# Optimization experiments

Hardware: AMD Instinct MI355X
Metric: run time of the kernel (lower is better)

Reference implementation:

```python
import jax, jax.numpy as jnp
import numpy as np
from jax import lax

BN_EPS = 1e-5
BNS = 1.0 / np.sqrt(1.0 + BN_EPS)  # eval-mode BatchNorm with mean=0, var=1, gamma=1, beta=0


def setup_inputs() -> dict:
    key = jax.random.key(0)
    ks = jax.random.split(key, 12)
    B, Cin, H, W = 8, 256, 128, 128
    NC, HD, RC, NL = 12, 64, 128, 3
    f = lambda k, shp, s: jax.random.normal(k, shp, jnp.float32) * s
    return dict(
        features=f(ks[0], (B, Cin, H, W), 1.0),
        segmentation=jax.random.uniform(ks[1], (B, NC, H, W), dtype=jnp.float32),
        W_rpn=f(ks[2], (RC, Cin, 3, 3), 0.02), b_rpn=jnp.zeros((RC,), jnp.float32),
        W_node=f(ks[3], (HD, RC), 0.08), b_node=jnp.zeros((HD,), jnp.float32),
        W_e1=f(ks[4], (2 * HD, HD), 0.08), b_e1=jnp.zeros((HD,), jnp.float32),
        W_e2=f(ks[5], (HD, HD), 0.1), b_e2=jnp.zeros((HD,), jnp.float32),
        W_g=f(ks[6], (NL, HD, HD), 0.1), b_g=jnp.zeros((NL, HD), jnp.float32),
        ln_g=jnp.ones((NL, HD), jnp.float32), ln_b=jnp.zeros((NL, HD), jnp.float32),
        glob_emb=f(ks[7], (NC, HD), 0.02),
        W_sp=f(ks[8], (HD, RC), 0.1), b_sp=jnp.zeros((RC,), jnp.float32),
    )


def _forward(features, segmentation, W_rpn, b_rpn, W_node, b_node, W_e1, b_e1,
             W_e2, b_e2, W_g, b_g, ln_g, ln_b, glob_emb, W_sp, b_sp):
    B, NC, H, W = segmentation.shape
    HD = W_node.shape[0]
    NL = W_g.shape[0]

    # ---- RegionProposalNetwork: 3x3 conv + BN(eval) + ReLU ----
    refined = lax.conv_general_dilated(
        features, W_rpn, (1, 1), 'SAME',
        dimension_numbers=('NCHW', 'OIHW', 'NCHW'))
    refined = jax.nn.relu((refined + b_rpn[None, :, None, None]) * BNS)  # [B,RC,H,W]

    # per-class 3x3 maxpool on segmentation, threshold -> binary masks
    pooled = lax.reduce_window(segmentation, -jnp.inf, lax.max,
                               (1, 1, 3, 3), (1, 1, 1, 1), 'SAME')
    masks = (pooled > 0.5).astype(features.dtype)  # [B,NC,H,W]

    # ---- NodeFeatureExtractor (1x1 conv is linear: conv(f*m)=(Wf)*m + b) ----
    yw = jnp.einsum('dk,bkhw->bdhw', W_node, refined)            # [B,HD,H,W]
    z = jax.nn.relu((yw + b_node[None, :, None, None]) * BNS)    # value inside mask region
    masked_sum = jnp.einsum('bdhw,bchw->bcd', z, masks)          # [B,NC,HD]
    mask_sum = masks.sum((2, 3))                                 # [B,NC]
    node_feats = masked_sum / (mask_sum[..., None] + 1e-6)       # [B,NC,HD]

    # ---- EdgeFeatureExtractor: all (i,j), i!=j, gated by class presence ----
    pairs = np.array([(i, j) for i in range(NC) for j in range(NC) if i != j])
    src = jnp.asarray(pairs[:, 0])  # [E]
    dst = jnp.asarray(pairs[:, 1])
    present = (mask_sum > 0).astype(features.dtype)              # [B,NC]
    valid = present[:, src] * present[:, dst]                    # [B,E]
    cat = jnp.concatenate([node_feats[:, src], node_feats[:, dst]], axis=-1)  # [B,E,2HD]
    h = jax.nn.relu(cat @ W_e1 + b_e1)
    edge_attr = (h @ W_e2 + b_e2) * valid[..., None]             # [B,E,HD]

    # ---- TissueGraphNetwork ----
    presence = (node_feats.sum(-1) != 0).astype(features.dtype)[..., None]  # [B,NC,1]
    seg_sum = jax.vmap(lambda m: jax.ops.segment_sum(m, dst, num_segments=NC))
    x = node_feats
    for l in range(NL):
        xw = x @ W_g[l]                                          # [B,NC,HD]
        msgs = xw[:, src] * edge_attr                            # [B,E,HD]
        agg = seg_sum(msgs) + b_g[l]
        xr = jax.nn.relu(agg)
        mu = xr.mean(-1, keepdims=True)
        var = ((xr - mu) ** 2).mean(-1, keepdims=True)
        normed = (xr - mu) / jnp.sqrt(var + 1e-5) * ln_g[l] + ln_b[l]
        x = normed + x if l > 0 else normed
    x = x * presence + glob_emb[None] * (1.0 - presence)         # [B,NC,HD]

    # ---- SpatialProjector ----
    spatial = jnp.einsum('bcd,bchw->bdhw', x, masks)             # [B,HD,H,W]
    out = jnp.einsum('do,bdhw->bohw', W_sp, spatial)             # [B,RC,H,W]
    out = jax.nn.relu((out + b_sp[None, :, None, None]) * BNS)
    return out


def reference(features, segmentation, W_rpn, b_rpn, W_node, b_node, W_e1, b_e1,
              W_e2, b_e2, W_g, b_g, ln_g, ln_b, glob_emb, W_sp, b_sp):
    return _forward(features, segmentation, W_rpn, b_rpn, W_node, b_node,
                    W_e1, b_e1, W_e2, b_e2, W_g, b_g, ln_g, ln_b,
                    glob_emb, W_sp, b_sp)
```

## Files before the change

kernel.cpp:

```cpp
#include <hip/hip_runtime.h>
#include <math.h>

#define BNS_F 0.9999950000374998f

typedef short short8 __attribute__((ext_vector_type(8)));
typedef float f32x16 __attribute__((ext_vector_type(16)));

typedef __attribute__((address_space(3))) void lds_void;
typedef const __attribute__((address_space(1))) void glb_void;

__device__ __forceinline__ unsigned short f2bf(float f) {
    unsigned u = __builtin_bit_cast(unsigned, f);
    unsigned r = (u + 0x7fffu + ((u >> 16) & 1u)) >> 16;
    return (unsigned short)r;
}
__device__ __forceinline__ float bf2f(unsigned short h) {
    unsigned u = ((unsigned)h) << 16;
    return __builtin_bit_cast(float, u);
}

__global__ __launch_bounds__(256) void prep_kernel(
    const float* __restrict__ feat, unsigned short* __restrict__ Fbt,
    const float* __restrict__ Wrpn, unsigned short* __restrict__ Wr,
    const float* __restrict__ seg, float* __restrict__ masks,
    float* __restrict__ mask_sum)
{
    int bid = blockIdx.x;
    int t = threadIdx.x;

    if (bid < 16384) {
        int pxc = bid & 63;
        int icg = (bid >> 6) & 31;
        int b   = bid >> 11;
        int px  = pxc * 256 + t;
        const float* src = feat + ((size_t)(b * 256 + icg * 8)) * 16384 + px;
        unsigned v[4];
        #pragma unroll
        for (int i = 0; i < 4; ++i) {
            unsigned lo = f2bf(src[(size_t)(2 * i)     * 16384]);
            unsigned hi = f2bf(src[(size_t)(2 * i + 1) * 16384]);
            v[i] = lo | (hi << 16);
        }
        uint4 o; o.x = v[0]; o.y = v[1]; o.z = v[2]; o.w = v[3];
        *(uint4*)(Fbt + (((size_t)(b * 32 + icg) * 16384) + px) * 8) = o;
    } else if (bid < 16512) {
        int oc = bid - 16384;
        const float* src = Wrpn + ((size_t)oc * 256 + t) * 9;
        #pragma unroll
        for (int tap = 0; tap < 9; ++tap)
            Wr[((size_t)tap * 128 + oc) * 256 + t] = f2bf(src[tap]);
    } else {
        int mb = bid - 16512;
        int h = (mb & 63) * 2 + (t >> 7);
        int c = (mb >> 6) % 12;
        int b = mb / (64 * 12);
        int px = t & 127;

        const float* s = seg + ((size_t)(b * 12 + c) * 128) * 128;
        float m = -INFINITY;
        #pragma unroll
        for (int dy = -1; dy <= 1; ++dy) {
            int y = h + dy;
            if (y < 0 || y > 127) continue;
            #pragma unroll
            for (int dx = -1; dx <= 1; ++dx) {
                int x = px + dx;
                if (x < 0 || x > 127) continue;
                m = fmaxf(m, s[y * 128 + x]);
            }
        }
        float v = (m > 0.5f) ? 1.0f : 0.0f;
        masks[((size_t)(b * 12 + c) * 128 + h) * 128 + px] = v;

        float cnt = v;
        #pragma unroll
        for (int off = 1; off < 64; off <<= 1) cnt += __shfl_xor(cnt, off, 64);
        if ((t & 63) == 0) atomicAdd(&mask_sum[b * 12 + c], cnt);
    }
}

#define BUF_BYTES 24960
#define CHUNK_STEP (4u * 16384u * 8u)

__global__ __launch_bounds__(512) void conv_node_kernel(
    const unsigned short* __restrict__ Fbt, const unsigned short* __restrict__ Wr,
    const float* __restrict__ brpn, const float* __restrict__ Wnode,
    const float* __restrict__ bnode, const float* __restrict__ masks,
    const float* __restrict__ zero16, float* __restrict__ ms_rep)
{
    __shared__ __align__(16) unsigned char lds[49920];

    int wg = blockIdx.x;
    int bid = (wg & 7) * 128 + (wg >> 3);
    int h = bid & 127, b = bid >> 7;

    int t = threadIdx.x;
    int lane = t & 63;
    int wv = __builtin_amdgcn_readfirstlane(t >> 6);
    int mw = wv >> 2;
    int nw = wv & 3;
    int ln31 = lane & 31;
    int khalf = lane >> 5;
    int px0 = nw * 32;

    f32x16 acc0 = (f32x16)0.f, acc1 = (f32x16)0.f;

    const unsigned short* zp = (const unsigned short*)zero16;

    const unsigned short* pp[4];
    unsigned inc[4];
    #pragma unroll
    for (int r = 0; r < 4; ++r) {
        int c = (r < 3) ? (r * 512 + t) : (1536 + t);
        bool act = (r < 3) || (t < 24);
        int row = c / 520;
        int rem = c - row * 520;
        int slot = rem / 130;
        int col = rem - slot * 130;
        int y = h - 1 + row, x = col - 1;
        bool in = act && ((unsigned)y < 128u) && ((unsigned)x < 128u);
        pp[r] = in ? (Fbt + (((size_t)(b * 32 + slot) * 16384) + y * 128 + x) * 8)
                   : zp;
        inc[r] = in ? CHUNK_STEP : 0u;
    }

    auto stage = [&](int bsel) {
        #pragma unroll
        for (int r = 0; r < 3; ++r) {
            unsigned ldsoff = (unsigned)bsel * BUF_BYTES
                            + (unsigned)(r * 512 + wv * 64) * 16;
            __builtin_amdgcn_global_load_lds((glb_void*)pp[r],
                (lds_void*)(lds + ldsoff), 16, 0, 0);
            pp[r] += inc[r];
        }
        if (t < 24) {
            unsigned ldsoff = (unsigned)bsel * BUF_BYTES + 1536u * 16;
            __builtin_amdgcn_global_load_lds((glb_void*)pp[3],
                (lds_void*)(lds + ldsoff), 16, 0, 0);
        }
        pp[3] += inc[3];
    };

    stage(0);
    __syncthreads();

    for (int s = 0; s < 8; ++s) {
        int ic0 = s * 32;
        const unsigned char* buf = lds + (s & 1) * BUF_BYTES;

        #pragma unroll
        for (int ks = 0; ks < 2; ++ks) {
            #pragma unroll
            for (int dy = 0; dy < 3; ++dy) {
                #pragma unroll
                for (int dxi = 0; dxi < 3; ++dxi) {
                    int tap = dy * 3 + dxi;
                    const unsigned short* wp = Wr
                        + ((size_t)(tap * 128 + mw * 64 + ln31) * 256
                           + ic0 + ks * 16 + khalf * 8);
                    short8 a0 = *(const short8*)wp;
                    short8 a1 = *(const short8*)(wp + 32 * 256);

                    unsigned off = (unsigned)dy * 8320u
                                 + (unsigned)(2 * ks + khalf) * 2080u
                                 + (unsigned)(px0 + ln31 + dxi) * 16u;
                    short8 bf = *(const short8*)(buf + off);

                    acc0 = __builtin_amdgcn_mfma_f32_32x32x16_bf16(
                        a0, bf, acc0, 0, 0, 0);
                    acc1 = __builtin_amdgcn_mfma_f32_32x32x16_bf16(
                        a1, bf, acc1, 0, 0, 0);
                }
            }
        }

        if (s < 7) stage((s + 1) & 1);
        __syncthreads();
    }

    unsigned short* refined = (unsigned short*)lds;
    int px = px0 + ln31;
    #pragma unroll
    for (int reg = 0; reg < 16; ++reg) {
        int row = (reg & 3) + 8 * (reg >> 2) + 4 * khalf;
        int oc0 = mw * 64 + row;
        float v0 = fmaxf((acc0[reg] + brpn[oc0]) * BNS_F, 0.f);
        refined[oc0 * 130 + px] = f2bf(v0);
        int oc1 = oc0 + 32;
        float v1 = fmaxf((acc1[reg] + brpn[oc1]) * BNS_F, 0.f);
        refined[oc1 * 130 + px] = f2bf(v1);
    }
    __syncthreads();

    float z0[8], z1[8];
    #pragma unroll
    for (int j = 0; j < 8; ++j) { z0[j] = 0.f; z1[j] = 0.f; }
    const float* wn = Wnode + (size_t)wv * 8 * 128;
    for (int k = 0; k < 128; ++k) {
        float r0 = bf2f(refined[k * 130 + lane]);
        float r1 = bf2f(refined[k * 130 + 64 + lane]);
        #pragma unroll
        for (int j = 0; j < 8; ++j) {
            float w = wn[j * 128 + k];
            z0[j] = fmaf(w, r0, z0[j]);
            z1[j] = fmaf(w, r1, z1[j]);
        }
    }
    #pragma unroll
    for (int j = 0; j < 8; ++j) {
        float bb = bnode[wv * 8 + j];
        z0[j] = fmaxf((z0[j] + bb) * BNS_F, 0.f);
        z1[j] = fmaxf((z1[j] + bb) * BNS_F, 0.f);
    }

    int rep = bid & 7;
    const float* mrow = masks + ((size_t)b * 12 * 128 + h) * 128;
    float* msb = ms_rep + ((size_t)(rep * 8 + b) * 12) * 64 + wv * 8;
    for (int c = 0; c < 12; ++c) {
        float m0 = mrow[(size_t)c * 16384 + lane];
        float m1 = mrow[(size_t)c * 16384 + 64 + lane];
        #pragma unroll
        for (int j = 0; j < 8; ++j) {
            float v = fmaf(z0[j], m0, z1[j] * m1);
            #pragma unroll
            for (int off2 = 1; off2 < 64; off2 <<= 1) v += __shfl_xor(v, off2, 64);
            if (lane == 0) atomicAdd(&msb[c * 64 + j], v);
        }
    }
}

__global__ __launch_bounds__(256) void edge_kernel(
    const float* __restrict__ ms_rep, const float* __restrict__ mask_sum,
    const float* __restrict__ We1, const float* __restrict__ be1,
    const float* __restrict__ We2, const float* __restrict__ be2,
    float* __restrict__ ea_g)
{
    int gb = blockIdx.x;
    int b = gb / 33, eg = gb % 33;
    int wv = threadIdx.x >> 6, d = threadIdx.x & 63;
    int e = eg * 4 + wv;
    int src = e / 11, jj = e % 11;
    int dst = jj + (jj >= src ? 1 : 0);

    float mssrc = 0.f, msdst = 0.f;
    #pragma unroll
    for (int rep = 0; rep < 8; ++rep) {
        mssrc += ms_rep[((size_t)(rep * 8 + b) * 12 + src) * 64 + d];
        msdst += ms_rep[((size_t)(rep * 8 + b) * 12 + dst) * 64 + d];
    }
    float cs = mask_sum[b * 12 + src], cd = mask_sum[b * 12 + dst];
    float nsrc = mssrc / (cs + 1e-6f);
    float ndst = msdst / (cd + 1e-6f);

    float hv = be1[d];
    for (int k = 0; k < 64; ++k) hv = fmaf(__shfl(nsrc, k, 64), We1[k * 64 + d], hv);
    for (int k = 0; k < 64; ++k) hv = fmaf(__shfl(ndst, k, 64), We1[(64 + k) * 64 + d], hv);
    hv = fmaxf(hv, 0.f);
    float av = be2[d];
    for (int k = 0; k < 64; ++k) av = fmaf(__shfl(hv, k, 64), We2[k * 64 + d], av);

    float valid = ((cs > 0.f) ? 1.f : 0.f) * ((cd > 0.f) ? 1.f : 0.f);
    ea_g[((size_t)b * 132 + e) * 64 + d] = av * valid;
}

__global__ __launch_bounds__(256) void graph_kernel(
    const float* __restrict__ ms_rep, const float* __restrict__ mask_sum,
    const float* __restrict__ ea_g,
    const float* __restrict__ Wg, const float* __restrict__ bg,
    const float* __restrict__ lng, const float* __restrict__ lnb,
    const float* __restrict__ glob, const float* __restrict__ Wsp,
    float* __restrict__ xs_out)
{
    __shared__ float nf[12 * 64];
    __shared__ float x [12 * 64];
    __shared__ float xw[12 * 64];
    __shared__ float ea[132 * 64];
    __shared__ float presence[12];

    int b = blockIdx.x;
    int t = threadIdx.x;

    for (int i = t; i < 768; i += 256) {
        int c = i >> 6, d = i & 63;
        float ms = 0.f;
        #pragma unroll
        for (int rep = 0; rep < 8; ++rep)
            ms += ms_rep[((size_t)(rep * 8 + b) * 12 + c) * 64 + d];
        nf[i] = ms / (mask_sum[b * 12 + c] + 1e-6f);
    }
    for (int i = t; i < 132 * 64; i += 256) ea[i] = ea_g[(size_t)b * 8448 + i];
    __syncthreads();

    for (int i = t; i < 768; i += 256) {
        int c = i >> 6;
        float v = nf[i];
        #pragma unroll
        for (int off = 1; off < 64; off <<= 1) v += __shfl_xor(v, off, 64);
        if ((i & 63) == 0) presence[c] = (v != 0.f) ? 1.f : 0.f;
        x[i] = nf[i];
    }
    __syncthreads();

    for (int l = 0; l < 3; ++l) {
        const float* wg = Wg + l * 4096;
        for (int i = t; i < 768; i += 256) {
            int c = i >> 6, d = i & 63;
            float v = 0.f;
            for (int k = 0; k < 64; ++k) v = fmaf(x[c * 64 + k], wg[k * 64 + d], v);
            xw[i] = v;
        }
        __syncthreads();
        for (int i = t; i < 768; i += 256) {
            int j = i >> 6, d = i & 63;
            float agg = bg[l * 64 + d];
            #pragma unroll
            for (int src2 = 0; src2 < 12; ++src2) {
                if (src2 == j) continue;
                int jj2 = j - (j > src2 ? 1 : 0);
                int e = src2 * 11 + jj2;
                agg = fmaf(xw[src2 * 64 + d], ea[e * 64 + d], agg);
            }
            float xr = fmaxf(agg, 0.f);
            float s = xr;
            #pragma unroll
            for (int off = 1; off < 64; off <<= 1) s += __shfl_xor(s, off, 64);
            float mu = s * (1.f / 64.f);
            float df = xr - mu;
            float s2 = df * df;
            #pragma unroll
            for (int off = 1; off < 64; off <<= 1) s2 += __shfl_xor(s2, off, 64);
            float var = s2 * (1.f / 64.f);
            float normed = df * (1.0f / sqrtf(var + 1e-5f)) * lng[l * 64 + d]
                           + lnb[l * 64 + d];
            nf[i] = (l > 0) ? (normed + x[i]) : normed;
        }
        __syncthreads();
        for (int i = t; i < 768; i += 256) x[i] = nf[i];
        __syncthreads();
    }

    for (int i = t; i < 768; i += 256) {
        int c = i >> 6;
        float p = presence[c];
        x[i] = x[i] * p + glob[c * 64 + (i & 63)] * (1.f - p);
    }
    __syncthreads();

    for (int i = t; i < 12 * 128; i += 256) {
        int c = i >> 7, o = i & 127;
        float v = 0.f;
        for (int k = 0; k < 64; ++k) v = fmaf(x[c * 64 + k], Wsp[k * 128 + o], v);
        xs_out[b * 1536 + i] = v;
    }
}

__global__ __launch_bounds__(256) void out_kernel(
    const float* __restrict__ xs, const float* __restrict__ masks,
    const float* __restrict__ bsp, float* __restrict__ out)
{
    __shared__ float xsl[12 * 128];
    __shared__ float ml[12 * 128];
    int bid = blockIdx.x;
    int h = bid & 127;
    int b = bid >> 7;
    int t = threadIdx.x;

    for (int i = t; i < 1536; i += 256) xsl[i] = xs[b * 1536 + i];
    for (int i = t; i < 1536; i += 256) {
        int c = i >> 7, px = i & 127;
        ml[i] = masks[((size_t)(b * 12 + c) * 128 + h) * 128 + px];
    }
    __syncthreads();

    int px = t & 127;
    int og = t >> 7;
    float m[12];
    #pragma unroll
    for (int c = 0; c < 12; ++c) m[c] = ml[c * 128 + px];

    float* ob = out + ((size_t)b * 128 * 128 + h) * 128 + px;
    for (int i = 0; i < 64; ++i) {
        int o = og * 64 + i;
        float s = 0.f;
        #pragma unroll
        for (int c = 0; c < 12; ++c) s = fmaf(xsl[c * 128 + o], m[c], s);
        ob[(size_t)o * 16384] = fmaxf((s + bsp[o]) * BNS_F, 0.f);
    }
}

extern "C" void kernel_launch(void* const* d_in, const int* in_sizes, int n_in,
                              void* d_out, int out_size, void* d_ws, size_t ws_size,
                              hipStream_t stream)
{
    const float* feat  = (const float*)d_in[0];
    const float* seg   = (const float*)d_in[1];
    const float* Wrpn  = (const float*)d_in[2];
    const float* brpn  = (const float*)d_in[3];
    const float* Wnode = (const float*)d_in[4];
    const float* bnode = (const float*)d_in[5];
    const float* We1   = (const float*)d_in[6];
    const float* be1   = (const float*)d_in[7];
    const float* We2   = (const float*)d_in[8];
    const float* be2   = (const float*)d_in[9];
    const float* Wg    = (const float*)d_in[10];
    const float* bg    = (const float*)d_in[11];
    const float* lng   = (const float*)d_in[12];
    const float* lnb   = (const float*)d_in[13];
    const float* glob  = (const float*)d_in[14];
    const float* Wsp   = (const float*)d_in[15];
    const float* bsp   = (const float*)d_in[16];
    float* out = (float*)d_out;

    unsigned short* Fbt = (unsigned short*)d_out;

    float* masks    = (float*)d_ws;
    float* ms_rep   = masks + 1572864;
    float* mask_sum = ms_rep + 49152;
    float* zero16   = mask_sum + 96;
    float* xs       = zero16 + 8;
    float* ea_g     = xs + 12288;
    unsigned short* Wr = (unsigned short*)(ea_g + 67584);

    hipMemsetAsync(ms_rep, 0, (49152 + 96 + 8) * sizeof(float), stream);

    prep_kernel<<<22656, 256, 0, stream>>>(feat, Fbt, Wrpn, Wr, seg, masks, mask_sum);
    conv_node_kernel<<<1024, 512, 0, stream>>>(Fbt, Wr, brpn, Wnode, bnode,
                                               masks, zero16, ms_rep);
    edge_kernel<<<264, 256, 0, stream>>>(ms_rep, mask_sum, We1, be1, We2, be2, ea_g);
    graph_kernel<<<8, 256, 0, stream>>>(ms_rep, mask_sum, ea_g,
                                        Wg, bg, lng, lnb, glob, Wsp, xs);
    out_kernel<<<1024, 256, 0, stream>>>(xs, masks, bsp, out);
}
```

Before: 566.2 us.

## Split conv rows into half-row tiles using 16x16x32 MFMA with smaller LDS

The conv+node kernel now processes half an image row (64 pixels) per workgroup instead of a full row, doubling the grid. It switches from 32x32x16 to 16x16x32 bf16 MFMA, with each wave owning 16 output channels across four 16-pixel tiles, and halves the LDS staging buffers. Launch bounds now request higher occupancy. The aim is more concurrent workgroups and better latency hiding. The cost is more halo reloads per pixel and more weight-fragment global loads per output.

```diff
diff --git a/kernel.cpp b/kernel.cpp
--- a/kernel.cpp
+++ b/kernel.cpp
@@ -4,7 +4,7 @@
 #define BNS_F 0.9999950000374998f
 
 typedef short short8 __attribute__((ext_vector_type(8)));
-typedef float f32x16 __attribute__((ext_vector_type(16)));
+typedef float f32x4 __attribute__((ext_vector_type(4)));
 
 typedef __attribute__((address_space(3))) void lds_void;
 typedef const __attribute__((address_space(1))) void glb_void;
@@ -79,97 +79,87 @@
     }
 }
 
-#define BUF_BYTES 24960
+#define BUF_B 12672
 #define CHUNK_STEP (4u * 16384u * 8u)
 
-__global__ __launch_bounds__(512) void conv_node_kernel(
+__global__ __launch_bounds__(512, 8) void conv_node_kernel(
     const unsigned short* __restrict__ Fbt, const unsigned short* __restrict__ Wr,
     const float* __restrict__ brpn, const float* __restrict__ Wnode,
     const float* __restrict__ bnode, const float* __restrict__ masks,
     const float* __restrict__ zero16, float* __restrict__ ms_rep)
 {
-    __shared__ __align__(16) unsigned char lds[49920];
+    __shared__ __align__(16) unsigned char lds[25344];
 
     int wg = blockIdx.x;
-    int bid = (wg & 7) * 128 + (wg >> 3);
-    int h = bid & 127, b = bid >> 7;
+    int bid = (wg & 7) * 256 + (wg >> 3);
+    int b    = bid >> 8;
+    int h    = (bid >> 1) & 127;
+    int px0  = (bid & 1) * 64;
 
     int t = threadIdx.x;
     int lane = t & 63;
     int wv = __builtin_amdgcn_readfirstlane(t >> 6);
-    int mw = wv >> 2;
-    int nw = wv & 3;
-    int ln31 = lane & 31;
-    int khalf = lane >> 5;
-    int px0 = nw * 32;
-
-    f32x16 acc0 = (f32x16)0.f, acc1 = (f32x16)0.f;
+    int kg = lane >> 4;
+    int ln15 = lane & 15;
+
+    f32x4 acc[4];
+    #pragma unroll
+    for (int nt = 0; nt < 4; ++nt) acc[nt] = (f32x4){0.f, 0.f, 0.f, 0.f};
 
     const unsigned short* zp = (const unsigned short*)zero16;
 
-    const unsigned short* pp[4];
-    unsigned inc[4];
-    #pragma unroll
-    for (int r = 0; r < 4; ++r) {
-        int c = (r < 3) ? (r * 512 + t) : (1536 + t);
-        bool act = (r < 3) || (t < 24);
-        int row = c / 520;
-        int rem = c - row * 520;
-        int slot = rem / 130;
-        int col = rem - slot * 130;
-        int y = h - 1 + row, x = col - 1;
+    const unsigned short* pp0;
+    const unsigned short* pp1;
+    #pragma unroll
+    for (int r = 0; r < 2; ++r) {
+        int c = r * 512 + t;
+        bool act = (c < 792);
+        int row = c / 264;
+        int rem = c - row * 264;
+        int slot = rem / 66;
+        int col = rem - slot * 66;
+        int y = h - 1 + row, x = px0 + col - 1;
         bool in = act && ((unsigned)y < 128u) && ((unsigned)x < 128u);
-        pp[r] = in ? (Fbt + (((size_t)(b * 32 + slot) * 16384) + y * 128 + x) * 8)
-                   : zp;
-        inc[r] = in ? CHUNK_STEP : 0u;
+        const unsigned short* p =
+            in ? (Fbt + (((size_t)(b * 32 + slot) * 16384) + y * 128 + x) * 8) : zp;
+        if (r == 0) pp0 = p; else pp1 = p;
     }
 
     auto stage = [&](int bsel) {
-        #pragma unroll
-        for (int r = 0; r < 3; ++r) {
-            unsigned ldsoff = (unsigned)bsel * BUF_BYTES
-                            + (unsigned)(r * 512 + wv * 64) * 16;
-            __builtin_amdgcn_global_load_lds((glb_void*)pp[r],
-                (lds_void*)(lds + ldsoff), 16, 0, 0);
-            pp[r] += inc[r];
-        }
-        if (t < 24) {
-            unsigned ldsoff = (unsigned)bsel * BUF_BYTES + 1536u * 16;
-            __builtin_amdgcn_global_load_lds((glb_void*)pp[3],
-                (lds_void*)(lds + ldsoff), 16, 0, 0);
-        }
-        pp[3] += inc[3];
+        unsigned lo0 = (unsigned)bsel * BUF_B + (unsigned)(wv * 64) * 16;
+        __builtin_amdgcn_global_load_lds((glb_void*)pp0,
+            (lds_void*)(lds + lo0), 16, 0, 0);
+        pp0 += (pp0 == zp) ? 0u : CHUNK_STEP;
+        if (512 + t < 792) {
+            unsigned lo1 = (unsigned)bsel * BUF_B + (unsigned)(512 + wv * 64) * 16;
+            __builtin_amdgcn_global_load_lds((glb_void*)pp1,
+                (lds_void*)(lds + lo1), 16, 0, 0);
+        }
+        pp1 += (pp1 == zp) ? 0u : CHUNK_STEP;
     };
 
+    unsigned vb = (unsigned)(kg * 66 + ln15) * 16;
+    unsigned laneA = (unsigned)(ln15 * 256 + kg * 8);
+
     stage(0);
     __syncthreads();
 
     for (int s = 0; s < 8; ++s) {
-        int ic0 = s * 32;
-        const unsigned char* buf = lds + (s & 1) * BUF_BYTES;
-
-        #pragma unroll
-        for (int ks = 0; ks < 2; ++ks) {
-            #pragma unroll
-            for (int dy = 0; dy < 3; ++dy) {
+        const unsigned short* wpu = Wr + (size_t)(wv * 16) * 256 + s * 32 + laneA;
+        unsigned bb = (unsigned)(s & 1) * BUF_B + vb;
+
+        #pragma unroll
+        for (int dy = 0; dy < 3; ++dy) {
+            #pragma unroll
+            for (int dxi = 0; dxi < 3; ++dxi) {
+                int tap = dy * 3 + dxi;
+                short8 a = *(const short8*)(wpu + (size_t)tap * 32768);
                 #pragma unroll
-                for (int dxi = 0; dxi < 3; ++dxi) {
-                    int tap = dy * 3 + dxi;
-                    const unsigned short* wp = Wr
-                        + ((size_t)(tap * 128 + mw * 64 + ln31) * 256
-                           + ic0 + ks * 16 + khalf * 8);
-                    short8 a0 = *(const short8*)wp;
-                    short8 a1 = *(const short8*)(wp + 32 * 256);
-
-                    unsigned off = (unsigned)dy * 8320u
-                                 + (unsigned)(2 * ks + khalf) * 2080u
-                                 + (unsigned)(px0 + ln31 + dxi) * 16u;
-                    short8 bf = *(const short8*)(buf + off);
-
-                    acc0 = __builtin_amdgcn_mfma_f32_32x32x16_bf16(
-                        a0, bf, acc0, 0, 0, 0);
-                    acc1 = __builtin_amdgcn_mfma_f32_32x32x16_bf16(
-                        a1, bf, acc1, 0, 0, 0);
+                for (int nt = 0; nt < 4; ++nt) {
+                    short8 bf = *(const short8*)
+                        (lds + bb + (unsigned)((dy * 264 + dxi) * 16 + nt * 256));
+                    acc[nt] = __builtin_amdgcn_mfma_f32_16x16x32_bf16(
+                        a, bf, acc[nt], 0, 0, 0);
                 }
             }
         }
@@ -179,52 +169,43 @@
     }
 
     unsigned short* refined = (unsigned short*)lds;
-    int px = px0 + ln31;
-    #pragma unroll
-    for (int reg = 0; reg < 16; ++reg) {
-        int row = (reg & 3) + 8 * (reg >> 2) + 4 * khalf;
-        int oc0 = mw * 64 + row;
-        float v0 = fmaxf((acc0[reg] + brpn[oc0]) * BNS_F, 0.f);
-        refined[oc0 * 130 + px] = f2bf(v0);
-        int oc1 = oc0 + 32;
-        float v1 = fmaxf((acc1[reg] + brpn[oc1]) * BNS_F, 0.f);
-        refined[oc1 * 130 + px] = f2bf(v1);
-    }
-    __syncthreads();
-
-    float z0[8], z1[8];
-    #pragma unroll
-    for (int j = 0; j < 8; ++j) { z0[j] = 0.f; z1[j] = 0.f; }
-    const float* wn = Wnode + (size_t)wv * 8 * 128;
+    #pragma unroll
+    for (int nt = 0; nt < 4; ++nt) {
+        #pragma unroll
+        for (int r = 0; r < 4; ++r) {
+            int oc = wv * 16 + kg * 4 + r;
+            int px = nt * 16 + ln15;
+            float v = fmaxf((acc[nt][r] + brpn[oc]) * BNS_F, 0.f);
+            refined[oc * 66 + px] = f2bf(v);
+        }
+    }
+    __syncthreads();
+
+    float z[8];
+    #pragma unroll
+    for (int j = 0; j < 8; ++j) z[j] = 0.f;
+    const float* wn = Wnode + (size_t)(wv * 8) * 128;
     for (int k = 0; k < 128; ++k) {
-        float r0 = bf2f(refined[k * 130 + lane]);
-        float r1 = bf2f(refined[k * 130 + 64 + lane]);
-        #pragma unroll
-        for (int j = 0; j < 8; ++j) {
-            float w = wn[j * 128 + k];
-            z0[j] = fmaf(w, r0, z0[j]);
-            z1[j] = fmaf(w, r1, z1[j]);
-        }
-    }
-    #pragma unroll
-    for (int j = 0; j < 8; ++j) {
-        float bb = bnode[wv * 8 + j];
-        z0[j] = fmaxf((z0[j] + bb) * BNS_F, 0.f);
-        z1[j] = fmaxf((z1[j] + bb) * BNS_F, 0.f);
-    }
+        float rv = bf2f(refined[k * 66 + lane]);
+        #pragma unroll
+        for (int j = 0; j < 8; ++j)
+            z[j] = fmaf(wn[j * 128 + k], rv, z[j]);
+    }
+    #pragma unroll
+    for (int j = 0; j < 8; ++j)
+        z[j] = fmaxf((z[j] + bnode[wv * 8 + j]) * BNS_F, 0.f);
 
     int rep = bid & 7;
-    const float* mrow = masks + ((size_t)b * 12 * 128 + h) * 128;
+    const float* mrow = masks + ((size_t)b * 12 * 128 + h) * 128 + px0;
     float* msb = ms_rep + ((size_t)(rep * 8 + b) * 12) * 64 + wv * 8;
     for (int c = 0; c < 12; ++c) {
-        float m0 = mrow[(size_t)c * 16384 + lane];
-        float m1 = mrow[(size_t)c * 16384 + 64 + lane];
+        float m = mrow[(size_t)c * 16384 + lane];
         #pragma unroll
         for (int j = 0; j < 8; ++j) {
-            float v = fmaf(z0[j], m0, z1[j] * m1);
+            float v = z[j] * m;
             #pragma unroll
             for (int off2 = 1; off2 < 64; off2 <<= 1) v += __shfl_xor(v, off2, 64);
-            if (lane == 0) atomicAdd(&msb[c * 64 + j], v);
+            if (lane == j) atomicAdd(&msb[c * 64 + j], v);
         }
     }
 }
@@ -424,7 +405,7 @@
     hipMemsetAsync(ms_rep, 0, (49152 + 96 + 8) * sizeof(float), stream);
 
     prep_kernel<<<22656, 256, 0, stream>>>(feat, Fbt, Wrpn, Wr, seg, masks, mask_sum);
-    conv_node_kernel<<<1024, 512, 0, stream>>>(Fbt, Wr, brpn, Wnode, bnode,
+    conv_node_kernel<<<2048, 512, 0, stream>>>(Fbt, Wr, brpn, Wnode, bnode,
                                                masks, zero16, ms_rep);
     edge_kernel<<<264, 256, 0, stream>>>(ms_rep, mask_sum, We1, be1, We2, be2, ea_g);
     graph_kernel<<<8, 256, 0, stream>>>(ms_rep, mask_sum, ea_g,
```

Result: faster. 468.9 us (-17.2%).
